# Kernel tuning notes

Hardware: AMD Instinct MI355X
Metric: run time of the kernel (lower is better)

The kernel has to match this reference:

```python
import jax, jax.numpy as jnp
import numpy as np

D = 512
H = 8
G = 4          # GroupNorm groups
EPS = 1e-3     # GroupNorm eps


def group_norm(x):
    # x: (b, n, t, d); torch code normalizes per (batch, group) over (n*t, d/G)
    b, n, t, d = x.shape
    xr = x.reshape(b, n * t, G, d // G)
    mu = xr.mean(axis=(1, 3), keepdims=True)
    var = ((xr - mu) ** 2).mean(axis=(1, 3), keepdims=True)
    return ((xr - mu) * jax.lax.rsqrt(var + EPS)).reshape(b, n, t, d)


def setup_inputs() -> dict:
    key = jax.random.key(0)
    ks = jax.random.split(key, 9)
    s = 1.0 / np.sqrt(D)
    inp = {
        "ind": 0,
        "in_f": jax.random.normal(ks[0], (4, 8, 512, D), dtype=jnp.float32),
        "in_f_kv": jax.random.normal(ks[1], (4, 8, 512, D), dtype=jnp.float32),
        "Wq": jax.random.normal(ks[2], (D, D), dtype=jnp.float32) * s,
        "Wk": jax.random.normal(ks[3], (D, D), dtype=jnp.float32) * s,
        "Wv": jax.random.normal(ks[4], (D, D), dtype=jnp.float32) * s,
        "Wz": jax.random.normal(ks[5], (D, D), dtype=jnp.float32) * s,
        "bz": jnp.zeros((D,), dtype=jnp.float32),
        "W1": jax.random.normal(ks[6], (D, D), dtype=jnp.float32) * s,
        "b1": jnp.full((D,), 0.1, dtype=jnp.float32),
        "W2": jax.random.normal(ks[7], (D, D), dtype=jnp.float32) * s,
        "b2": jnp.full((D,), 0.1, dtype=jnp.float32),
    }
    return inp


def reference(ind, in_f, in_f_kv, Wq, Wk, Wv, Wz, bz, W1, b1, W2, b2):
    b, n, t, d = in_f.shape
    hd = d // H
    scale = 1.0 / np.sqrt(hd)

    _in_f = group_norm(in_f)          # LN_1
    _in_f_kv = group_norm(in_f_kv)    # LN_2

    # torch Linear: y = x @ W.T
    q = group_norm(_in_f @ Wq.T)      # LN_3
    k = group_norm(_in_f_kv @ Wk.T)   # LN_4
    v = _in_f_kv @ Wv.T

    q = q.reshape(b, n, t, H, hd)
    k = k.reshape(b, n, -1, H, hd)
    v = v.reshape(b, n, -1, H, hd)

    logits = jnp.einsum('bnqhd,bnkhd->bnhqk', q, k) * scale
    attn_weights = jax.nn.softmax(logits, axis=-1)
    attn_out = jnp.einsum('bnhqk,bnkhd->bnqhd', attn_weights, v).reshape(b, n, t, d)

    in_f_u1 = attn_out @ Wz.T + bz
    in_f_u2 = jax.nn.leaky_relu(_in_f @ W1.T + b1, negative_slope=0.01) @ W2.T + b2

    out_f = in_f + in_f_u1 + in_f_u2
    return (out_f, attn_weights)
```

## Files before the change

kernel.cpp:

```cpp
#include <hip/hip_runtime.h>
#include <math.h>

#define TDIM 512
#define DDIM 512
#define NTROWS 4096
#define MROWS 16384
#define EPSGN 1e-3f

typedef __attribute__((ext_vector_type(8))) short bf16x8;
typedef __attribute__((ext_vector_type(4))) float f32x4;
typedef __attribute__((ext_vector_type(8))) unsigned short us8;
typedef __attribute__((ext_vector_type(4))) unsigned short us4;

__device__ __forceinline__ unsigned short f2b(float f) {
  unsigned int u = __float_as_uint(f);
  return (unsigned short)((u + 0x7fffu + ((u >> 16) & 1u)) >> 16);
}
__device__ __forceinline__ float b2f(unsigned short h) {
  return __uint_as_float(((unsigned int)h) << 16);
}

#define GLOAD16(g, l)                                                                   \
  __builtin_amdgcn_global_load_lds((const __attribute__((address_space(1))) void*)(g),  \
                                   (__attribute__((address_space(3))) void*)(l), 16, 0, 0)

__global__ __launch_bounds__(256) void stats_cvt(const float* __restrict__ x0,
                                                 const float* __restrict__ x1,
                                                 unsigned short* __restrict__ o0,
                                                 unsigned short* __restrict__ o1,
                                                 float* __restrict__ p0,
                                                 float* __restrict__ p1,
                                                 const float* __restrict__ Wz,
                                                 const float* __restrict__ W2,
                                                 unsigned short* __restrict__ w16s) {
  if (blockIdx.y == 2) {
    const int bid = blockIdx.x;
    if (bid >= 256) return;
    const int c = bid * 256 + threadIdx.x;
    const int t = c >> 15;
    const int off = c & 32767;
    const float* s = t ? W2 : Wz;
    unsigned short* d = w16s + (size_t)(16 + t) * 262144;
    const float4 f0 = *(const float4*)(s + (size_t)off * 8);
    const float4 f1 = *(const float4*)(s + (size_t)off * 8 + 4);
    us8 v;
    v[0] = f2b(f0.x); v[1] = f2b(f0.y); v[2] = f2b(f0.z); v[3] = f2b(f0.w);
    v[4] = f2b(f1.x); v[5] = f2b(f1.y); v[6] = f2b(f1.z); v[7] = f2b(f1.w);
    *(us8*)(d + (size_t)off * 8) = v;
    return;
  }
  const float* x = blockIdx.y ? x1 : x0;
  unsigned short* o = blockIdx.y ? o1 : o0;
  float* part = blockIdx.y ? p1 : p0;
  const int blk = blockIdx.x;
  const int batch = blk >> 7;
  const int chunk = blk & 127;
  const size_t base = (size_t)blk * 32 * 512;
  const int tid = threadIdx.x;
  float s = 0.f, sq = 0.f;
#pragma unroll 4
  for (int it = 0; it < 8; ++it) {
    const size_t e = base + (size_t)it * 2048 + (size_t)tid * 8;
    const float4 f0 = *(const float4*)(x + e);
    const float4 f1 = *(const float4*)(x + e + 4);
    us8 v;
    v[0] = f2b(f0.x); v[1] = f2b(f0.y); v[2] = f2b(f0.z); v[3] = f2b(f0.w);
    v[4] = f2b(f1.x); v[5] = f2b(f1.y); v[6] = f2b(f1.z); v[7] = f2b(f1.w);
    *(us8*)(o + e) = v;
    s += f0.x + f0.y + f0.z + f0.w + f1.x + f1.y + f1.z + f1.w;
    sq += f0.x * f0.x + f0.y * f0.y + f0.z * f0.z + f0.w * f0.w +
          f1.x * f1.x + f1.y * f1.y + f1.z * f1.z + f1.w * f1.w;
  }
  const int wave = tid >> 6, lane = tid & 63;
#pragma unroll
  for (int of = 1; of < 16; of <<= 1) { s += __shfl_xor(s, of); sq += __shfl_xor(sq, of); }
  __shared__ float red[4][4][2];
  if ((lane & 15) == 0) { red[wave][lane >> 4][0] = s; red[wave][lane >> 4][1] = sq; }
  __syncthreads();
  if (tid < 4) {
    float S = 0.f, SQ = 0.f;
#pragma unroll
    for (int w = 0; w < 4; ++w) { S += red[w][tid][0]; SQ += red[w][tid][1]; }
    const int idx = (((batch << 2) | tid) << 7) | chunk;
    part[idx * 2] = S;
    part[idx * 2 + 1] = SQ;
  }
}

__global__ __launch_bounds__(256) void wprep(const float* __restrict__ Wq,
                                             const float* __restrict__ Wk,
                                             const float* __restrict__ Wv,
                                             const float* __restrict__ W1,
                                             const float* __restrict__ p0,
                                             const float* __restrict__ p1,
                                             unsigned short* __restrict__ w16s,
                                             float* __restrict__ corr) {
  const int y = blockIdx.y;
  const int w = y >> 2, b = y & 3;
  const float* W = (w == 0) ? Wq : (w == 1) ? Wk : (w == 2) ? Wv : W1;
  const float* part = (w == 0 || w == 3) ? p0 : p1;
  __shared__ float mrs[4][2];
  if (threadIdx.x < 4) {
    const float* p = part + (((b << 2) | threadIdx.x) << 7) * 2;
    float S = 0.f, SQ = 0.f;
    for (int c = 0; c < 128; ++c) { S += p[c * 2]; SQ += p[c * 2 + 1]; }
    const float inv = 1.f / (float)(NTROWS * 128);
    const float mu = S * inv;
    const float var = SQ * inv - mu * mu;
    const float rs = rsqrtf(var + EPSGN);
    mrs[threadIdx.x][0] = rs;
    mrs[threadIdx.x][1] = mu * rs;
  }
  __syncthreads();
  const int wave = threadIdx.x >> 6, lane = threadIdx.x & 63;
  const int n = blockIdx.x * 4 + wave;
  const int k = lane * 8;
  const int g = lane >> 4;
  const float rs = mrs[g][0], murs = mrs[g][1];
  const float4 f0 = *(const float4*)(W + (size_t)n * 512 + k);
  const float4 f1 = *(const float4*)(W + (size_t)n * 512 + k + 4);
  us8 v;
  v[0] = f2b(f0.x * rs); v[1] = f2b(f0.y * rs); v[2] = f2b(f0.z * rs); v[3] = f2b(f0.w * rs);
  v[4] = f2b(f1.x * rs); v[5] = f2b(f1.y * rs); v[6] = f2b(f1.z * rs); v[7] = f2b(f1.w * rs);
  *(us8*)(w16s + (size_t)((w << 2) | b) * 262144 + (size_t)n * 512 + k) = v;
  float t = (f0.x + f0.y + f0.z + f0.w + f1.x + f1.y + f1.z + f1.w) * murs;
#pragma unroll
  for (int of = 1; of < 64; of <<= 1) t += __shfl_xor(t, of);
  if (lane == 0) corr[(((w << 2) | b) << 9) | n] = t;
}

__global__ __launch_bounds__(256) void gemm_all(const unsigned short* __restrict__ a16,
                                                const unsigned short* __restrict__ akv16,
                                                const unsigned short* __restrict__ w16s,
                                                const float* __restrict__ corr,
                                                unsigned short* __restrict__ q16,
                                                unsigned short* __restrict__ h16,
                                                unsigned short* __restrict__ k16,
                                                unsigned short* __restrict__ vTb,
                                                const float* __restrict__ b1,
                                                float* __restrict__ part_q,
                                                float* __restrict__ part_k,
                                                float* __restrict__ sk) {
  __shared__ __align__(16) unsigned short As[128 * 64];
  __shared__ __align__(16) unsigned short Bs[128 * 64];
  __shared__ float red[8];
  const int tid = threadIdx.x;
  const int wave = tid >> 6, lane = tid & 63;
  const int bm = blockIdx.x << 7;
  const int batch = blockIdx.x >> 5;
  const int z = blockIdx.z;
  const bool first = blockIdx.y < 4;
  const int widx = z ? (first ? 1 : 2) : (first ? 0 : 3);
  const unsigned short* A = z ? akv16 : a16;
  const unsigned short* B = w16s + (size_t)262144 * ((widx << 2) | batch);
  const int bnl = (blockIdx.y & 3) << 7;
  const int wr = (wave >> 1) << 6;
  const int wc = (wave & 1) << 6;
  const int lr = lane & 15, lg = lane >> 4;

  f32x4 acc[4][4] = {};
  const int srow = lane >> 3;
  const int sslot = (lane & 7) ^ srow;

  for (int k0 = 0; k0 < 512; k0 += 64) {
    __syncthreads();
#pragma unroll
    for (int i = 0; i < 4; ++i) {
      const int ci = wave * 4 + i;
      const int row = ci * 8 + srow;
      GLOAD16(A + (size_t)(bm + row) * 512 + k0 + sslot * 8, (char*)As + ci * 1024);
      GLOAD16(B + (size_t)(bnl + row) * 512 + k0 + sslot * 8, (char*)Bs + ci * 1024);
    }
    __syncthreads();
#pragma unroll
    for (int kk = 0; kk < 64; kk += 32) {
      bf16x8 af[4], bfr[4];
#pragma unroll
      for (int i = 0; i < 4; ++i) {
        const int row = wr + i * 16 + lr;
        af[i] = *(const bf16x8*)&As[row * 64 + ((((kk >> 3) + lg) ^ (row & 7)) << 3)];
      }
#pragma unroll
      for (int j = 0; j < 4; ++j) {
        const int row = wc + j * 16 + lr;
        bfr[j] = *(const bf16x8*)&Bs[row * 64 + ((((kk >> 3) + lg) ^ (row & 7)) << 3)];
      }
#pragma unroll
      for (int i = 0; i < 4; ++i)
#pragma unroll
        for (int j = 0; j < 4; ++j)
          acc[i][j] = __builtin_amdgcn_mfma_f32_16x16x32_bf16(af[i], bfr[j], acc[i][j], 0, 0, 0);
    }
  }

  {
    const float* cb = corr + (((widx << 2) | batch) << 9);
    float cj[4];
#pragma unroll
    for (int j = 0; j < 4; ++j) cj[j] = cb[bnl + wc + j * 16 + lr];
#pragma unroll
    for (int i = 0; i < 4; ++i)
#pragma unroll
      for (int j = 0; j < 4; ++j)
#pragma unroll
        for (int r = 0; r < 4; ++r) acc[i][j][r] -= cj[j];
  }

  if (first) {
    unsigned short* C0 = z ? k16 : q16;
#pragma unroll
    for (int i = 0; i < 4; ++i) {
      const int row0 = bm + wr + i * 16 + lg * 4;
#pragma unroll
      for (int j = 0; j < 4; ++j) {
        const int col = bnl + wc + j * 16 + lr;
#pragma unroll
        for (int r = 0; r < 4; ++r)
          C0[(size_t)(row0 + r) * 512 + col] = f2b(acc[i][j][r]);
      }
    }
    float s = 0.f, sq = 0.f;
#pragma unroll
    for (int i = 0; i < 4; ++i)
#pragma unroll
      for (int j = 0; j < 4; ++j)
#pragma unroll
        for (int r = 0; r < 4; ++r) { const float v = acc[i][j][r]; s += v; sq += v * v; }
#pragma unroll
    for (int o = 32; o > 0; o >>= 1) { s += __shfl_xor(s, o); sq += __shfl_xor(sq, o); }
    if (lane == 0) { red[wave * 2] = s; red[wave * 2 + 1] = sq; }
    __syncthreads();
    if (tid == 0) {
      float* part = z ? part_k : part_q;
      const float S = red[0] + red[2] + red[4] + red[6];
      const float SQ = red[1] + red[3] + red[5] + red[7];
      const int slot = blockIdx.x & 31, g = blockIdx.y;
      const int idx = ((((batch << 2) | g) << 5) | slot) << 1;
      part[idx] = S;
      part[idx + 1] = SQ;
    }
    if (z) {
      const int head = (bnl >> 6) + (wave & 1);
#pragma unroll
      for (int i = 0; i < 4; ++i) {
#pragma unroll
        for (int r = 0; r < 4; ++r) {
          float t = acc[i][0][r] + acc[i][1][r] + acc[i][2][r] + acc[i][3][r];
#pragma unroll
          for (int o = 1; o < 16; o <<= 1) t += __shfl_xor(t, o);
          if (lr == 0)
            sk[(size_t)(bm + wr + i * 16 + lg * 4 + r) * 8 + head] = t;
        }
      }
    }
  } else if (z == 0) {
#pragma unroll
    for (int i = 0; i < 4; ++i) {
      const int row0 = bm + wr + i * 16 + lg * 4;
#pragma unroll
      for (int j = 0; j < 4; ++j) {
        const int col = bnl + wc + j * 16 + lr;
        const float bb = b1[col];
#pragma unroll
        for (int r = 0; r < 4; ++r) {
          float v = acc[i][j][r] + bb;
          v = v > 0.f ? v : 0.01f * v;
          h16[(size_t)(row0 + r) * 512 + col] = f2b(v);
        }
      }
    }
  } else {
#pragma unroll
    for (int i = 0; i < 4; ++i) {
      const int row0 = bm + wr + i * 16 + lg * 4;
#pragma unroll
      for (int j = 0; j < 4; ++j) {
        const int col = bnl + wc + j * 16 + lr;
        us4 pk;
#pragma unroll
        for (int r = 0; r < 4; ++r) pk[r] = f2b(acc[i][j][r]);
        *(us4*)&vTb[((size_t)(row0 >> 9) * 512 + col) * 512 + (row0 & 511)] = pk;
      }
    }
  }
}

__global__ __launch_bounds__(256) void gemm_final(const unsigned short* __restrict__ A0,
                                                  const unsigned short* __restrict__ A1,
                                                  const unsigned short* __restrict__ B0,
                                                  const unsigned short* __restrict__ B1,
                                                  float* __restrict__ Cf,
                                                  const float* __restrict__ bias0,
                                                  const float* __restrict__ bias1,
                                                  const unsigned short* __restrict__ init16) {
  __shared__ __align__(16) unsigned short As[128 * 64];
  __shared__ __align__(16) unsigned short Bs[128 * 64];
  const int tid = threadIdx.x;
  const int wave = tid >> 6, lane = tid & 63;
  const int bm = blockIdx.x << 7, bn = blockIdx.y << 7;
  const int wr = (wave >> 1) << 6;
  const int wc = (wave & 1) << 6;
  const int lr = lane & 15, lg = lane >> 4;

  f32x4 acc[4][4] = {};
  const int srow = lane >> 3;
  const int sslot = (lane & 7) ^ srow;

  for (int k0 = 0; k0 < 1024; k0 += 64) {
    const unsigned short* Ab = (k0 < 512) ? A0 : A1;
    const unsigned short* Bb = (k0 < 512) ? B0 : B1;
    const int kl = k0 & 511;
    __syncthreads();
#pragma unroll
    for (int i = 0; i < 4; ++i) {
      const int ci = wave * 4 + i;
      const int row = ci * 8 + srow;
      GLOAD16(Ab + (size_t)(bm + row) * 512 + kl + sslot * 8, (char*)As + ci * 1024);
      GLOAD16(Bb + (size_t)(bn + row) * 512 + kl + sslot * 8, (char*)Bs + ci * 1024);
    }
    __syncthreads();
#pragma unroll
    for (int kk = 0; kk < 64; kk += 32) {
      bf16x8 af[4], bfr[4];
#pragma unroll
      for (int i = 0; i < 4; ++i) {
        const int row = wr + i * 16 + lr;
        af[i] = *(const bf16x8*)&As[row * 64 + ((((kk >> 3) + lg) ^ (row & 7)) << 3)];
      }
#pragma unroll
      for (int j = 0; j < 4; ++j) {
        const int row = wc + j * 16 + lr;
        bfr[j] = *(const bf16x8*)&Bs[row * 64 + ((((kk >> 3) + lg) ^ (row & 7)) << 3)];
      }
#pragma unroll
      for (int i = 0; i < 4; ++i)
#pragma unroll
        for (int j = 0; j < 4; ++j)
          acc[i][j] = __builtin_amdgcn_mfma_f32_16x16x32_bf16(af[i], bfr[j], acc[i][j], 0, 0, 0);
    }
  }

#pragma unroll
  for (int i = 0; i < 4; ++i) {
    const int row0 = bm + wr + i * 16 + lg * 4;
#pragma unroll
    for (int j = 0; j < 4; ++j) {
      const int col = bn + wc + j * 16 + lr;
      const float bb = bias0[col] + bias1[col];
#pragma unroll
      for (int r = 0; r < 4; ++r) {
        const size_t o = (size_t)(row0 + r) * 512 + col;
        Cf[o] = acc[i][j][r] + bb + b2f(init16[o]);
      }
    }
  }
}

__global__ __launch_bounds__(256) void attn_fused(const unsigned short* __restrict__ q16,
                                                  const unsigned short* __restrict__ k16,
                                                  const unsigned short* __restrict__ vT,
                                                  const float* __restrict__ part_q,
                                                  const float* __restrict__ part_k,
                                                  const float* __restrict__ sk,
                                                  float* __restrict__ aw,
                                                  unsigned short* __restrict__ ao16) {
  __shared__ __align__(16) unsigned short Qs[64 * 64];
  __shared__ __align__(16) unsigned short Ks[256 * 64];
  __shared__ __align__(16) unsigned short Ps[64 * 256];
  __shared__ float WM[4][64];
  __shared__ float WS[4][64];
  __shared__ float sk_lds[512];
  __shared__ float cst[2];

  const int bid = blockIdx.x;
  const int q0 = blockIdx.y << 6;
  const int h = bid & 7;
  const int b = bid >> 6;
  const int tid = threadIdx.x;
  const int w = tid >> 6, lane = tid & 63;
  const int lr = lane & 15, lg = lane >> 4;
  const int srow = lane >> 3;
  const int sslot = (lane & 7) ^ srow;

  const size_t hb = (size_t)(bid >> 3) * (512 * 512);
  const unsigned short* Qg = q16 + hb + h * 64;
  const unsigned short* Kg = k16 + hb + h * 64;
  const unsigned short* Vg = vT + hb + (size_t)h * 64 * 512;

  if (tid == 0) {
    const int pbase = (((b << 2) | (h >> 1)) << 6);
    const float* pq = part_q + pbase;
    const float* pk = part_k + pbase;
    float Sq = 0.f, SQq = 0.f, Sk = 0.f, SQk = 0.f;
    for (int c = 0; c < 32; ++c) {
      Sq += pq[c * 2]; SQq += pq[c * 2 + 1];
      Sk += pk[c * 2]; SQk += pk[c * 2 + 1];
    }
    const float inv = 1.f / (float)(NTROWS * 128);
    const float muq = Sq * inv, vq = SQq * inv - muq * muq;
    const float muk = Sk * inv, vk = SQk * inv - muk * muk;
    const float a = rsqrtf(vq + EPSGN) * rsqrtf(vk + EPSGN) * 0.125f;
    cst[0] = a;
    cst[1] = a * muq;
  }
  {
    const float* skg = sk + (size_t)(bid >> 3) * 512 * 8 + h;
    for (int j = tid; j < 512; j += 256) sk_lds[j] = skg[(size_t)j * 8];
  }

#pragma unroll
  for (int it = 0; it < 2; ++it) {
    const int ci = w * 2 + it;
    const int row = ci * 8 + srow;
    GLOAD16(Qg + (size_t)(q0 + row) * 512 + sslot * 8, (char*)Qs + ci * 1024);
  }

  f32x4 sc[4][8] = {};

#pragma unroll
  for (int half = 0; half < 2; ++half) {
    __syncthreads();
#pragma unroll
    for (int it = 0; it < 8; ++it) {
      const int ci = w * 8 + it;
      const int row = ci * 8 + srow;
      GLOAD16(Kg + (size_t)(half * 256 + row) * 512 + sslot * 8, (char*)Ks + ci * 1024);
    }
    __syncthreads();
#pragma unroll
    for (int kk = 0; kk < 64; kk += 32) {
      bf16x8 aq[4];
#pragma unroll
      for (int qf = 0; qf < 4; ++qf) {
        const int row = qf * 16 + lr;
        aq[qf] = *(const bf16x8*)&Qs[row * 64 + ((((kk >> 3) + lg) ^ (row & 7)) << 3)];
      }
#pragma unroll
      for (int kf = 0; kf < 4; ++kf) {
        const int row = w * 64 + kf * 16 + lr;
        const bf16x8 bk = *(const bf16x8*)&Ks[row * 64 + ((((kk >> 3) + lg) ^ (row & 7)) << 3)];
#pragma unroll
        for (int qf = 0; qf < 4; ++qf)
          sc[qf][half * 4 + kf] =
              __builtin_amdgcn_mfma_f32_16x16x32_bf16(aq[qf], bk, sc[qf][half * 4 + kf], 0, 0, 0);
      }
    }
  }

#pragma unroll
  for (int it = 0; it < 8; ++it) {
    const int ci = w * 8 + it;
    const int row = ci * 2 + (lane >> 5);
    const int s = lane & 31;
    GLOAD16(Vg + (size_t)row * 512 + ((s ^ (row & 7)) << 3), (char*)Ks + ci * 1024);
  }

  const float aSc = cst[0], cmu = cst[1];
#pragma unroll
  for (int qf = 0; qf < 4; ++qf)
#pragma unroll
    for (int kfi = 0; kfi < 8; ++kfi) {
      const int k = ((kfi >> 2) << 8) + w * 64 + ((kfi & 3) << 4) + lr;
      const float corr = cmu * sk_lds[k];
#pragma unroll
      for (int r = 0; r < 4; ++r) sc[qf][kfi][r] = aSc * sc[qf][kfi][r] - corr;
    }

  float Mv[4][4];
#pragma unroll
  for (int qf = 0; qf < 4; ++qf)
#pragma unroll
    for (int r = 0; r < 4; ++r) {
      float m = sc[qf][0][r];
#pragma unroll
      for (int kf = 1; kf < 8; ++kf) m = fmaxf(m, sc[qf][kf][r]);
#pragma unroll
      for (int o = 1; o < 16; o <<= 1) m = fmaxf(m, __shfl_xor(m, o));
      Mv[qf][r] = m;
    }
  if (lr == 0) {
#pragma unroll
    for (int qf = 0; qf < 4; ++qf)
#pragma unroll
      for (int r = 0; r < 4; ++r) WM[w][qf * 16 + lg * 4 + r] = Mv[qf][r];
  }
  __syncthreads();
#pragma unroll
  for (int qf = 0; qf < 4; ++qf)
#pragma unroll
    for (int r = 0; r < 4; ++r) {
      const int q = qf * 16 + lg * 4 + r;
      Mv[qf][r] = fmaxf(fmaxf(WM[0][q], WM[1][q]), fmaxf(WM[2][q], WM[3][q]));
    }
  float sl[4][4] = {};
#pragma unroll
  for (int qf = 0; qf < 4; ++qf)
#pragma unroll
    for (int kf = 0; kf < 8; ++kf) {
      f32x4 v = sc[qf][kf];
#pragma unroll
      for (int r = 0; r < 4; ++r) {
        const float e = __expf(v[r] - Mv[qf][r]);
        v[r] = e;
        sl[qf][r] += e;
      }
      sc[qf][kf] = v;
    }
#pragma unroll
  for (int qf = 0; qf < 4; ++qf)
#pragma unroll
    for (int r = 0; r < 4; ++r) {
      float s = sl[qf][r];
#pragma unroll
      for (int o = 1; o < 16; o <<= 1) s += __shfl_xor(s, o);
      sl[qf][r] = s;
    }
  if (lr == 0) {
#pragma unroll
    for (int qf = 0; qf < 4; ++qf)
#pragma unroll
      for (int r = 0; r < 4; ++r) WS[w][qf * 16 + lg * 4 + r] = sl[qf][r];
  }
  __syncthreads();
#pragma unroll
  for (int qf = 0; qf < 4; ++qf)
#pragma unroll
    for (int r = 0; r < 4; ++r) {
      const int q = qf * 16 + lg * 4 + r;
      const float inv = 1.f / (WS[0][q] + WS[1][q] + WS[2][q] + WS[3][q]);
#pragma unroll
      for (int kf = 0; kf < 8; ++kf) sc[qf][kf][r] *= inv;
    }

  float* AWp = aw + ((size_t)bid * 512 + q0) * 512;
#pragma unroll
  for (int qf = 0; qf < 4; ++qf)
#pragma unroll
    for (int kfi = 0; kfi < 8; ++kfi) {
      const int k = ((kfi >> 2) << 8) + w * 64 + ((kfi & 3) << 4) + lr;
#pragma unroll
      for (int r = 0; r < 4; ++r)
        __builtin_nontemporal_store(sc[qf][kfi][r],
                                    &AWp[(size_t)(qf * 16 + lg * 4 + r) * 512 + k]);
    }

#pragma unroll
  for (int qf = 0; qf < 4; ++qf)
#pragma unroll
    for (int r = 0; r < 4; ++r) {
      const int q = qf * 16 + lg * 4 + r;
#pragma unroll
      for (int kf = 0; kf < 4; ++kf) {
        const int k = w * 64 + (kf << 4) + lr;
        Ps[q * 256 + (((k >> 3) ^ (q & 7)) << 3) + (k & 7)] = f2b(sc[qf][kf][r]);
      }
    }
  __syncthreads();

  f32x4 accO[4] = {};
#pragma unroll
  for (int ks = 0; ks < 256; ks += 32) {
    const int sl0 = ks >> 3;
    const int q = w * 16 + lr;
    const bf16x8 af = *(const bf16x8*)&Ps[q * 256 + (((sl0 + lg) ^ (q & 7)) << 3)];
#pragma unroll
    for (int df = 0; df < 4; ++df) {
      const int row = df * 16 + lr;
      const bf16x8 vb = *(const bf16x8*)&Ks[row * 256 + (((sl0 + lg) ^ (row & 7)) << 3)];
      accO[df] = __builtin_amdgcn_mfma_f32_16x16x32_bf16(af, vb, accO[df], 0, 0, 0);
    }
  }
  __syncthreads();

#pragma unroll
  for (int it = 0; it < 8; ++it) {
    const int ci = w * 8 + it;
    const int row = ci * 2 + (lane >> 5);
    const int s = lane & 31;
    GLOAD16(Vg + (size_t)row * 512 + 256 + ((s ^ (row & 7)) << 3), (char*)Ks + ci * 1024);
  }
#pragma unroll
  for (int qf = 0; qf < 4; ++qf)
#pragma unroll
    for (int r = 0; r < 4; ++r) {
      const int q = qf * 16 + lg * 4 + r;
#pragma unroll
      for (int kf = 0; kf < 4; ++kf) {
        const int k = w * 64 + (kf << 4) + lr;
        Ps[q * 256 + (((k >> 3) ^ (q & 7)) << 3) + (k & 7)] = f2b(sc[qf][4 + kf][r]);
      }
    }
  __syncthreads();

#pragma unroll
  for (int ks = 0; ks < 256; ks += 32) {
    const int sl0 = ks >> 3;
    const int q = w * 16 + lr;
    const bf16x8 af = *(const bf16x8*)&Ps[q * 256 + (((sl0 + lg) ^ (q & 7)) << 3)];
#pragma unroll
    for (int df = 0; df < 4; ++df) {
      const int row = df * 16 + lr;
      const bf16x8 vb = *(const bf16x8*)&Ks[row * 256 + (((sl0 + lg) ^ (row & 7)) << 3)];
      accO[df] = __builtin_amdgcn_mfma_f32_16x16x32_bf16(af, vb, accO[df], 0, 0, 0);
    }
  }

  const int growb = (bid >> 3) * 512 + q0 + w * 16 + lg * 4;
#pragma unroll
  for (int df = 0; df < 4; ++df)
#pragma unroll
    for (int r = 0; r < 4; ++r)
      ao16[(size_t)(growb + r) * 512 + h * 64 + df * 16 + lr] = f2b(accO[df][r]);
}

extern "C" void kernel_launch(void* const* d_in, const int* in_sizes, int n_in,
                              void* d_out, int out_size, void* d_ws, size_t ws_size,
                              hipStream_t stream) {
  const float* in_f = (const float*)d_in[1];
  const float* in_fkv = (const float*)d_in[2];
  const float* Wq = (const float*)d_in[3];
  const float* Wk = (const float*)d_in[4];
  const float* Wv = (const float*)d_in[5];
  const float* Wz = (const float*)d_in[6];
  const float* bz = (const float*)d_in[7];
  const float* W1 = (const float*)d_in[8];
  const float* b1 = (const float*)d_in[9];
  const float* W2 = (const float*)d_in[10];
  const float* b2 = (const float*)d_in[11];

  float* out_f = (float*)d_out;
  float* attw = out_f + (size_t)MROWS * DDIM;

  const size_t TSB = (size_t)MROWS * DDIM;
  unsigned short* us = (unsigned short*)d_ws;
  unsigned short* a16 = us;
  unsigned short* akv16 = us + TSB;
  unsigned short* q16 = us + 2 * TSB;
  unsigned short* k16 = us + 3 * TSB;
  unsigned short* h16 = us + 4 * TSB;
  unsigned short* ao16 = us + 5 * TSB;
  unsigned short* vT = us + 6 * TSB;
  unsigned short* w16s = us + 7 * TSB;
  float* fbase = (float*)(us + 7 * TSB + 18 * 262144);
  float* p0 = fbase;
  float* p1 = fbase + 4096;
  float* part_q = fbase + 8192;
  float* part_k = fbase + 9216;
  float* corr = fbase + 10240;
  float* sk = fbase + 18432;

  stats_cvt<<<dim3(512, 3), 256, 0, stream>>>(in_f, in_fkv, a16, akv16, p0, p1, Wz, W2, w16s);
  wprep<<<dim3(128, 16), 256, 0, stream>>>(Wq, Wk, Wv, W1, p0, p1, w16s, corr);
  gemm_all<<<dim3(128, 8, 2), 256, 0, stream>>>(a16, akv16, w16s, corr, q16, h16, k16, vT, b1,
                                                part_q, part_k, sk);
  attn_fused<<<dim3(256, 8), 256, 0, stream>>>(q16, k16, vT, part_q, part_k, sk, attw, ao16);
  gemm_final<<<dim3(128, 4), 256, 0, stream>>>(ao16, h16, w16s + 16 * 262144,
                                               w16s + 17 * 262144, out_f, bz, b2, a16);
}
```

Measured before the change: 239.1 us.

## Shrink attention LDS tiles to 128 keys to raise occupancy

The fused attention kernel now streams K and V through a single 128-row LDS tile in four steps instead of two 256-row halves, and the P staging buffer shrinks to 64x128. Probabilities are normalized once and converted to bf16 registers up front, then written to LDS per step. A launch bound of three blocks per CU is added. The aim is to cut LDS use so more blocks fit per CU and hide latency, at the cost of more barriers, smaller per-step loads, and register pressure from holding the packed bf16 probabilities.

```diff
diff --git a/kernel.cpp b/kernel.cpp
--- a/kernel.cpp
+++ b/kernel.cpp
@@ -356,17 +356,17 @@
   }
 }
 
-__global__ __launch_bounds__(256) void attn_fused(const unsigned short* __restrict__ q16,
-                                                  const unsigned short* __restrict__ k16,
-                                                  const unsigned short* __restrict__ vT,
-                                                  const float* __restrict__ part_q,
-                                                  const float* __restrict__ part_k,
-                                                  const float* __restrict__ sk,
-                                                  float* __restrict__ aw,
-                                                  unsigned short* __restrict__ ao16) {
+__global__ __launch_bounds__(256, 3) void attn_fused(const unsigned short* __restrict__ q16,
+                                                     const unsigned short* __restrict__ k16,
+                                                     const unsigned short* __restrict__ vT,
+                                                     const float* __restrict__ part_q,
+                                                     const float* __restrict__ part_k,
+                                                     const float* __restrict__ sk,
+                                                     float* __restrict__ aw,
+                                                     unsigned short* __restrict__ ao16) {
   __shared__ __align__(16) unsigned short Qs[64 * 64];
-  __shared__ __align__(16) unsigned short Ks[256 * 64];
-  __shared__ __align__(16) unsigned short Ps[64 * 256];
+  __shared__ __align__(16) unsigned short KVt[128 * 64];
+  __shared__ __align__(16) unsigned short Ps[64 * 128];
   __shared__ float WM[4][64];
   __shared__ float WS[4][64];
   __shared__ float sk_lds[512];
@@ -416,15 +416,14 @@
   }
 
   f32x4 sc[4][8] = {};
-
-#pragma unroll
-  for (int half = 0; half < 2; ++half) {
-    __syncthreads();
-#pragma unroll
-    for (int it = 0; it < 8; ++it) {
-      const int ci = w * 8 + it;
+#pragma unroll
+  for (int t = 0; t < 4; ++t) {
+    __syncthreads();
+#pragma unroll
+    for (int i = 0; i < 4; ++i) {
+      const int ci = w * 4 + i;
       const int row = ci * 8 + srow;
-      GLOAD16(Kg + (size_t)(half * 256 + row) * 512 + sslot * 8, (char*)Ks + ci * 1024);
+      GLOAD16(Kg + (size_t)(t * 128 + row) * 512 + sslot * 8, (char*)KVt + ci * 1024);
     }
     __syncthreads();
 #pragma unroll
@@ -436,34 +435,26 @@
         aq[qf] = *(const bf16x8*)&Qs[row * 64 + ((((kk >> 3) + lg) ^ (row & 7)) << 3)];
       }
 #pragma unroll
-      for (int kf = 0; kf < 4; ++kf) {
-        const int row = w * 64 + kf * 16 + lr;
-        const bf16x8 bk = *(const bf16x8*)&Ks[row * 64 + ((((kk >> 3) + lg) ^ (row & 7)) << 3)];
+      for (int kf = 0; kf < 2; ++kf) {
+        const int rl = w * 32 + kf * 16 + lr;
+        const bf16x8 bk = *(const bf16x8*)&KVt[rl * 64 + ((((kk >> 3) + lg) ^ (rl & 7)) << 3)];
 #pragma unroll
         for (int qf = 0; qf < 4; ++qf)
-          sc[qf][half * 4 + kf] =
-              __builtin_amdgcn_mfma_f32_16x16x32_bf16(aq[qf], bk, sc[qf][half * 4 + kf], 0, 0, 0);
-      }
-    }
-  }
-
-#pragma unroll
-  for (int it = 0; it < 8; ++it) {
-    const int ci = w * 8 + it;
-    const int row = ci * 2 + (lane >> 5);
-    const int s = lane & 31;
-    GLOAD16(Vg + (size_t)row * 512 + ((s ^ (row & 7)) << 3), (char*)Ks + ci * 1024);
+          sc[qf][t * 2 + kf] =
+              __builtin_amdgcn_mfma_f32_16x16x32_bf16(aq[qf], bk, sc[qf][t * 2 + kf], 0, 0, 0);
+      }
+    }
   }
 
   const float aSc = cst[0], cmu = cst[1];
 #pragma unroll
   for (int qf = 0; qf < 4; ++qf)
 #pragma unroll
-    for (int kfi = 0; kfi < 8; ++kfi) {
-      const int k = ((kfi >> 2) << 8) + w * 64 + ((kfi & 3) << 4) + lr;
+    for (int s = 0; s < 8; ++s) {
+      const int k = ((s >> 1) << 7) + w * 32 + ((s & 1) << 4) + lr;
       const float corr = cmu * sk_lds[k];
 #pragma unroll
-      for (int r = 0; r < 4; ++r) sc[qf][kfi][r] = aSc * sc[qf][kfi][r] - corr;
+      for (int r = 0; r < 4; ++r) sc[qf][s][r] = aSc * sc[qf][s][r] - corr;
     }
 
   float Mv[4][4];
@@ -522,86 +513,64 @@
       for (int r = 0; r < 4; ++r) WS[w][qf * 16 + lg * 4 + r] = sl[qf][r];
   }
   __syncthreads();
-#pragma unroll
-  for (int qf = 0; qf < 4; ++qf)
+
+  us4 pc[4][8];
+  float* AWp = aw + ((size_t)bid * 512 + q0) * 512;
+#pragma unroll
+  for (int qf = 0; qf < 4; ++qf) {
+    float inv[4];
 #pragma unroll
     for (int r = 0; r < 4; ++r) {
       const int q = qf * 16 + lg * 4 + r;
-      const float inv = 1.f / (WS[0][q] + WS[1][q] + WS[2][q] + WS[3][q]);
-#pragma unroll
-      for (int kf = 0; kf < 8; ++kf) sc[qf][kf][r] *= inv;
-    }
-
-  float* AWp = aw + ((size_t)bid * 512 + q0) * 512;
-#pragma unroll
-  for (int qf = 0; qf < 4; ++qf)
-#pragma unroll
-    for (int kfi = 0; kfi < 8; ++kfi) {
-      const int k = ((kfi >> 2) << 8) + w * 64 + ((kfi & 3) << 4) + lr;
-#pragma unroll
-      for (int r = 0; r < 4; ++r)
-        __builtin_nontemporal_store(sc[qf][kfi][r],
-                                    &AWp[(size_t)(qf * 16 + lg * 4 + r) * 512 + k]);
-    }
-
-#pragma unroll
-  for (int qf = 0; qf < 4; ++qf)
-#pragma unroll
-    for (int r = 0; r < 4; ++r) {
-      const int q = qf * 16 + lg * 4 + r;
-#pragma unroll
-      for (int kf = 0; kf < 4; ++kf) {
-        const int k = w * 64 + (kf << 4) + lr;
-        Ps[q * 256 + (((k >> 3) ^ (q & 7)) << 3) + (k & 7)] = f2b(sc[qf][kf][r]);
-      }
-    }
-  __syncthreads();
+      inv[r] = 1.f / (WS[0][q] + WS[1][q] + WS[2][q] + WS[3][q]);
+    }
+#pragma unroll
+    for (int s = 0; s < 8; ++s) {
+      const int k = ((s >> 1) << 7) + w * 32 + ((s & 1) << 4) + lr;
+#pragma unroll
+      for (int r = 0; r < 4; ++r) {
+        const float v = sc[qf][s][r] * inv[r];
+        __builtin_nontemporal_store(v, &AWp[(size_t)(qf * 16 + lg * 4 + r) * 512 + k]);
+        pc[qf][s][r] = f2b(v);
+      }
+    }
+  }
 
   f32x4 accO[4] = {};
 #pragma unroll
-  for (int ks = 0; ks < 256; ks += 32) {
-    const int sl0 = ks >> 3;
-    const int q = w * 16 + lr;
-    const bf16x8 af = *(const bf16x8*)&Ps[q * 256 + (((sl0 + lg) ^ (q & 7)) << 3)];
-#pragma unroll
-    for (int df = 0; df < 4; ++df) {
-      const int row = df * 16 + lr;
-      const bf16x8 vb = *(const bf16x8*)&Ks[row * 256 + (((sl0 + lg) ^ (row & 7)) << 3)];
-      accO[df] = __builtin_amdgcn_mfma_f32_16x16x32_bf16(af, vb, accO[df], 0, 0, 0);
-    }
-  }
-  __syncthreads();
-
-#pragma unroll
-  for (int it = 0; it < 8; ++it) {
-    const int ci = w * 8 + it;
-    const int row = ci * 2 + (lane >> 5);
-    const int s = lane & 31;
-    GLOAD16(Vg + (size_t)row * 512 + 256 + ((s ^ (row & 7)) << 3), (char*)Ks + ci * 1024);
-  }
-#pragma unroll
-  for (int qf = 0; qf < 4; ++qf)
-#pragma unroll
-    for (int r = 0; r < 4; ++r) {
-      const int q = qf * 16 + lg * 4 + r;
-#pragma unroll
-      for (int kf = 0; kf < 4; ++kf) {
-        const int k = w * 64 + (kf << 4) + lr;
-        Ps[q * 256 + (((k >> 3) ^ (q & 7)) << 3) + (k & 7)] = f2b(sc[qf][4 + kf][r]);
-      }
-    }
-  __syncthreads();
-
-#pragma unroll
-  for (int ks = 0; ks < 256; ks += 32) {
-    const int sl0 = ks >> 3;
-    const int q = w * 16 + lr;
-    const bf16x8 af = *(const bf16x8*)&Ps[q * 256 + (((sl0 + lg) ^ (q & 7)) << 3)];
-#pragma unroll
-    for (int df = 0; df < 4; ++df) {
-      const int row = df * 16 + lr;
-      const bf16x8 vb = *(const bf16x8*)&Ks[row * 256 + (((sl0 + lg) ^ (row & 7)) << 3)];
-      accO[df] = __builtin_amdgcn_mfma_f32_16x16x32_bf16(af, vb, accO[df], 0, 0, 0);
+  for (int t = 0; t < 4; ++t) {
+    __syncthreads();
+#pragma unroll
+    for (int i = 0; i < 4; ++i) {
+      const int ci = w * 4 + i;
+      const int row = ci * 4 + (lane >> 4);
+      const int s = lane & 15;
+      GLOAD16(Vg + (size_t)row * 512 + t * 128 + ((s ^ (row & 7)) << 3),
+              (char*)KVt + ci * 1024);
+    }
+#pragma unroll
+    for (int qf = 0; qf < 4; ++qf)
+#pragma unroll
+      for (int r = 0; r < 4; ++r) {
+        const int q = qf * 16 + lg * 4 + r;
+#pragma unroll
+        for (int kf = 0; kf < 2; ++kf) {
+          const int kl = w * 32 + kf * 16 + lr;
+          Ps[q * 128 + (((kl >> 3) ^ (q & 7)) << 3) + (kl & 7)] = pc[qf][t * 2 + kf][r];
+        }
+      }
+    __syncthreads();
+#pragma unroll
+    for (int ks = 0; ks < 128; ks += 32) {
+      const int q = w * 16 + lr;
+      const bf16x8 af = *(const bf16x8*)&Ps[q * 128 + ((((ks >> 3) + lg) ^ (q & 7)) << 3)];
+#pragma unroll
+      for (int df = 0; df < 4; ++df) {
+        const int vrow = df * 16 + lr;
+        const bf16x8 vb =
+            *(const bf16x8*)&KVt[vrow * 128 + ((((ks >> 3) + lg) ^ (vrow & 7)) << 3)];
+        accO[df] = __builtin_amdgcn_mfma_f32_16x16x32_bf16(af, vb, accO[df], 0, 0, 0);
+      }
     }
   }
 
```

Result: slower. 279.1 us (+16.7%).
